# Performance work log

Hardware: AMD Instinct MI355X
Metric: run time of the kernel (lower is better)

Reference implementation:

```python
import jax, jax.numpy as jnp
import numpy as np

B, T, C, H = 4, 2048, 1024, 16
D = C // H  # head dim = 64


def setup_inputs() -> dict:
    key = jax.random.key(0)
    ks = jax.random.split(key, 8)
    s = 1.0 / np.sqrt(C)
    return {
        "x": jax.random.normal(ks[0], (B, T, C), jnp.float32),
        "mask": jax.random.randint(ks[1], (B, T), 0, 2, jnp.int32),
        "Wq": jax.random.normal(ks[2], (C, C), jnp.float32) * s,
        "bq": jnp.zeros((C,), jnp.float32),
        "Wk": jax.random.normal(ks[3], (C, C), jnp.float32) * s,
        "bk": jnp.zeros((C,), jnp.float32),
        "Wv": jax.random.normal(ks[4], (C, C), jnp.float32) * s,
        "bv": jnp.zeros((C,), jnp.float32),
    }


def reference(x, mask, Wq, bq, Wk, bk, Wv, bv):
    # QKV projections (nn.Linear: x @ W.T + b); W stored here as [out,in] -> use W.T
    q = x @ Wq.T + bq
    k = x @ Wk.T + bk
    v = x @ Wv.T + bv
    # split heads: [B,T,C] -> [B,H,T,D]
    q = q.reshape(B, T, H, D).transpose(0, 2, 1, 3)
    k = k.reshape(B, T, H, D).transpose(0, 2, 1, 3)
    v = v.reshape(B, T, H, D).transpose(0, 2, 1, 3)
    # scaled dot-product attention scores [B,H,T,T]
    attn = jnp.einsum("bhqd,bhkd->bhqk", q, k) / jnp.sqrt(jnp.float32(D))
    # additive mask over key positions: attn - inf*(1-mask), expressed stably
    big_neg = jnp.float32(-1e30)
    attn = jnp.where(mask[:, None, None, :] > 0, attn, big_neg)
    attn = jax.nn.softmax(attn, axis=-1)
    # dropout p=0 -> identity
    y = jnp.einsum("bhqk,bhkd->bhqd", attn, v)
    # merge heads: [B,H,T,D] -> [B,T,C]
    return y.transpose(0, 2, 1, 3).reshape(B, T, C)
```

## Files before the change

### kernel.cpp

```cpp
#include <hip/hip_runtime.h>
#include <stdint.h>

#define BB 4
#define TT 2048
#define CC 1024
#define HH 16
#define DD 64
#define MM (BB * TT)

typedef unsigned short u16;
typedef unsigned int   u32;
typedef __attribute__((ext_vector_type(8))) short short8;
typedef _Float16 half8  __attribute__((ext_vector_type(8)));
typedef __fp16   fp16x2 __attribute__((ext_vector_type(2)));
typedef __attribute__((ext_vector_type(4))) float f32x4;
typedef __attribute__((ext_vector_type(4))) unsigned short u16x4;

#if __has_builtin(__builtin_amdgcn_exp2f)
#define EXP2(x) __builtin_amdgcn_exp2f(x)
#else
#define EXP2(x) __expf(0.69314718055994531f * (x))
#endif

__device__ inline u16 f2bf(float f) {
    union { float f; unsigned u; } v; v.f = f;
    unsigned r = 0x7fffu + ((v.u >> 16) & 1u);
    return (u16)((v.u + r) >> 16);
}
__device__ inline u16 f2h(float f) {
    union { _Float16 h; u16 u; } c; c.h = (_Float16)f; return c.u;
}
__device__ inline u32 pkh(float a, float b) {
    union { fp16x2 h; u32 u; } c;
    c.h = __builtin_amdgcn_cvt_pkrtz(a, b);
    return c.u;
}

#define NX (MM * CC / 4)
#define NW (CC * CC / 4)
__global__ void cvt_all(const float* __restrict__ x,  const float* __restrict__ Wq,
                        const float* __restrict__ Wk, const float* __restrict__ Wv,
                        u16* __restrict__ xb, u16* __restrict__ Wb) {
    int i = blockIdx.x * blockDim.x + threadIdx.x;
    const float* src; u16* dst; int j;
    if (i < NX)               { src = x;  dst = xb;                       j = i; }
    else if (i < NX + NW)     { src = Wq; dst = Wb;                       j = i - NX; }
    else if (i < NX + 2 * NW) { src = Wk; dst = Wb + (size_t)CC * CC;     j = i - NX - NW; }
    else if (i < NX + 3 * NW) { src = Wv; dst = Wb + (size_t)2 * CC * CC; j = i - NX - 2 * NW; }
    else return;
    float4 v = ((const float4*)src)[j];
    u16x4 o;
    o.x = f2bf(v.x); o.y = f2bf(v.y); o.z = f2bf(v.z); o.w = f2bf(v.w);
    ((u16x4*)dst)[j] = o;
}

__global__ void qkv_gemm(const u16* __restrict__ xb, const u16* __restrict__ Wb,
                         const float* __restrict__ bq, const float* __restrict__ bk,
                         const float* __restrict__ bv,
                         u16* __restrict__ Qh, u16* __restrict__ Kh, u16* __restrict__ Vt)
{
    const int z = blockIdx.z;
    const u16* W = Wb + (size_t)z * CC * CC;
    const float* bias = (z == 0) ? bq : ((z == 1) ? bk : bv);
    const float scale = (z == 0) ? 0.18033688011112042f : 1.0f;

    __shared__ __align__(16) u16 As[128][32];
    __shared__ __align__(16) u16 Bs[128][32];

    const int tid = threadIdx.x;
    const int l  = tid & 63, w = tid >> 6;
    const int wm = w >> 1,  wn = w & 1;
    const int lr = l & 15,  lq = l >> 4;
    const int m0 = blockIdx.y * 128, n0 = blockIdx.x * 128;

    f32x4 acc[4][4] = {};

    for (int kt = 0; kt < CC; kt += 32) {
        __syncthreads();
        #pragma unroll
        for (int r = 0; r < 2; ++r) {
            int c   = (r * 4 + w) * 64 + l;
            int row = c >> 2, kc = c & 3;
            const u16* ga = xb + (size_t)(m0 + row) * CC + kt + kc * 8;
            __builtin_amdgcn_global_load_lds(
                (const __attribute__((address_space(1))) void*)ga,
                (__attribute__((address_space(3))) void*)(&As[0][0] + (size_t)c * 8), 16, 0, 0);
            const u16* gb = W + (size_t)(n0 + row) * CC + kt + kc * 8;
            __builtin_amdgcn_global_load_lds(
                (const __attribute__((address_space(1))) void*)gb,
                (__attribute__((address_space(3))) void*)(&Bs[0][0] + (size_t)c * 8), 16, 0, 0);
        }
        __syncthreads();

        short8 af[4], bfr[4];
        #pragma unroll
        for (int mi = 0; mi < 4; ++mi)
            af[mi] = *(const short8*)&As[wm * 64 + mi * 16 + lr][lq * 8];
        #pragma unroll
        for (int ni = 0; ni < 4; ++ni)
            bfr[ni] = *(const short8*)&Bs[wn * 64 + ni * 16 + lr][lq * 8];
        #pragma unroll
        for (int mi = 0; mi < 4; ++mi)
            #pragma unroll
            for (int ni = 0; ni < 4; ++ni)
                acc[mi][ni] = __builtin_amdgcn_mfma_f32_16x16x32_bf16(
                    af[mi], bfr[ni], acc[mi][ni], 0, 0, 0);
    }

    if (z == 2) {
        #pragma unroll
        for (int ni = 0; ni < 4; ++ni) {
            int n = n0 + wn * 64 + ni * 16 + lr;
            float bvv = bias[n];
            int h = n >> 6, d = n & 63;
            #pragma unroll
            for (int mi = 0; mi < 4; ++mi) {
                int mbase = m0 + wm * 64 + mi * 16 + lq * 4;
                int b = mbase >> 11, t0 = mbase & (TT - 1);
                u16x4 pkv;
                #pragma unroll
                for (int r = 0; r < 4; ++r)
                    pkv[r] = f2h(acc[mi][ni][r] + bvv);
                *(u16x4*)&Vt[((size_t)(b * HH + h) * DD + d) * TT + t0] = pkv;
            }
        }
    } else {
        u16* out = (z == 0) ? Qh : Kh;
        #pragma unroll
        for (int ni = 0; ni < 4; ++ni) {
            int n = n0 + wn * 64 + ni * 16 + lr;
            float bvv = bias[n];
            int h = n >> 6, d = n & 63;
            #pragma unroll
            for (int mi = 0; mi < 4; ++mi) {
                int mbase = m0 + wm * 64 + mi * 16 + lq * 4;
                #pragma unroll
                for (int r = 0; r < 4; ++r) {
                    int m = mbase + r;
                    int b = m >> 11, t = m & (TT - 1);
                    out[((size_t)(b * HH + h) * TT + t) * DD + d] =
                        f2h((acc[mi][ni][r] + bvv) * scale);
                }
            }
        }
    }
}

__global__ __launch_bounds__(256, 4)
void attn_kernel(const u16* __restrict__ Qh, const u16* __restrict__ Kh,
                 const u16* __restrict__ Vt, const int* __restrict__ mask,
                 float* __restrict__ out)
{
    const int qt = blockIdx.x;
    const int h  = blockIdx.y;
    const int b  = blockIdx.z;
    const int tid = threadIdx.x;
    const int l  = tid & 63, w = tid >> 6;
    const int lr = l & 15,  lq = l >> 4;

    __shared__ __align__(16) u16 Ks[2][2][32][40];
    __shared__ __align__(16) u16 Vs[2][80][40];
    __shared__ __align__(16) u16 Ps[4][32][40];

    const size_t base = (size_t)(b * HH + h) * TT * DD;
    const int q0 = qt * 128 + w * 32;

    half8 qf[2][2];
    #pragma unroll
    for (int qi = 0; qi < 2; ++qi)
        #pragma unroll
        for (int kc = 0; kc < 2; ++kc)
            qf[qi][kc] = *(const half8*)(Qh + base + (size_t)(q0 + qi * 16 + lr) * DD
                                         + kc * 32 + lq * 8);

    const int kk  = tid >> 3, dc = tid & 7;
    const int kh  = dc >> 2, kck = dc & 3;
    const int krow = (kk & 1) * 16 + (kk >> 1);
    u16* k_dst0 = &Ks[0][kh][krow][kck * 8];
    const u16* k_base = Kh + base + (size_t)kk * DD + dc * 8;
    const int vd = tid >> 2, vck = tid & 3;
    u16* v_dst0 = &Vs[0][vd][vck * 8];
    const u16* v_base = Vt + base + (size_t)vd * TT + vck * 8;
    const int2* mrow = (const int2*)(mask + b * TT);

    #pragma unroll
    for (int i = tid; i < 16 * 40; i += 256) {
        (&Vs[0][64][0])[i] = 0x3C00;
        (&Vs[1][64][0])[i] = 0x3C00;
    }

    *(half8*)k_dst0 = *(const half8*)k_base;
    *(half8*)v_dst0 = *(const half8*)v_base;

    f32x4 o[2][5] = {};

    const int NT = TT / 32;
    __syncthreads();

    for (int kt = 0; kt < NT; ++kt) {
        const int p = kt & 1;
        int ktn = (kt + 1 < NT) ? kt + 1 : NT - 1;
        half8 kreg = *(const half8*)(k_base + (size_t)ktn * 32 * DD);
        half8 vreg = *(const half8*)(v_base + ktn * 32);
        int2 mm = mrow[kt * 16 + lr];
        float f0 = (float)mm.x, f1 = (float)mm.y;

        const u16 (*Kp)[32][40] = Ks[p];
        half8 k00 = *(const half8*)&Kp[0][lr][lq * 8];
        half8 k01 = *(const half8*)&Kp[1][lr][lq * 8];
        half8 k10 = *(const half8*)&Kp[0][16 + lr][lq * 8];
        half8 k11 = *(const half8*)&Kp[1][16 + lr][lq * 8];
        f32x4 s0[2], s1[2];
        #pragma unroll
        for (int qi = 0; qi < 2; ++qi) {
            f32x4 z0 = {}, z1 = {};
            z0 = __builtin_amdgcn_mfma_f32_16x16x32_f16(qf[qi][0], k00, z0, 0, 0, 0);
            z0 = __builtin_amdgcn_mfma_f32_16x16x32_f16(qf[qi][1], k01, z0, 0, 0, 0);
            z1 = __builtin_amdgcn_mfma_f32_16x16x32_f16(qf[qi][0], k10, z1, 0, 0, 0);
            z1 = __builtin_amdgcn_mfma_f32_16x16x32_f16(qf[qi][1], k11, z1, 0, 0, 0);
            s0[qi] = z0; s1[qi] = z1;
        }

        #pragma unroll
        for (int qi = 0; qi < 2; ++qi)
            #pragma unroll
            for (int r = 0; r < 4; ++r) {
                float pe = EXP2(s0[qi][r]) * f0;
                float po = EXP2(s1[qi][r]) * f1;
                *(u32*)&Ps[w][qi * 16 + lq * 4 + r][2 * lr] = pkh(pe, po);
            }
        __builtin_amdgcn_sched_barrier(0);
        half8 pf0 = *(const half8*)&Ps[w][lr][lq * 8];
        half8 pf1 = *(const half8*)&Ps[w][16 + lr][lq * 8];

        #pragma unroll
        for (int dg = 0; dg < 5; ++dg) {
            half8 vf = *(const half8*)&Vs[p][dg * 16 + lr][lq * 8];
            o[0][dg] = __builtin_amdgcn_mfma_f32_16x16x32_f16(pf0, vf, o[0][dg], 0, 0, 0);
            o[1][dg] = __builtin_amdgcn_mfma_f32_16x16x32_f16(pf1, vf, o[1][dg], 0, 0, 0);
        }

        *(half8*)(k_dst0 + (p ^ 1) * (2 * 32 * 40)) = kreg;
        *(half8*)(v_dst0 + (p ^ 1) * (80 * 40)) = vreg;
        __syncthreads();
    }

    #pragma unroll
    for (int qi = 0; qi < 2; ++qi)
        #pragma unroll
        for (int r = 0; r < 4; ++r) {
            float inv = 1.f / o[qi][4][r];
            int t = q0 + qi * 16 + lq * 4 + r;
            float* op = out + (size_t)(b * TT + t) * CC + h * DD;
            #pragma unroll
            for (int dg = 0; dg < 4; ++dg)
                op[dg * 16 + lr] = o[qi][dg][r] * inv;
        }
}

extern "C" void kernel_launch(void* const* d_in, const int* in_sizes, int n_in,
                              void* d_out, int out_size, void* d_ws, size_t ws_size,
                              hipStream_t stream) {
    const float* x    = (const float*)d_in[0];
    const int*   mask = (const int*)d_in[1];
    const float* Wq   = (const float*)d_in[2];
    const float* bq   = (const float*)d_in[3];
    const float* Wk   = (const float*)d_in[4];
    const float* bk   = (const float*)d_in[5];
    const float* Wv   = (const float*)d_in[6];
    const float* bv   = (const float*)d_in[7];
    float* out = (float*)d_out;

    u16* xb = (u16*)d_ws;
    u16* Wb = xb + (size_t)MM * CC;
    u16* Qh = Wb + (size_t)3 * CC * CC;
    u16* Kh = Qh + (size_t)MM * CC;
    u16* Vt = Kh + (size_t)MM * CC;

    {
        int total = NX + 3 * NW;
        cvt_all<<<(total + 255) / 256, 256, 0, stream>>>(x, Wq, Wk, Wv, xb, Wb);
    }

    qkv_gemm<<<dim3(CC / 128, MM / 128, 3), 256, 0, stream>>>(xb, Wb, bq, bk, bv, Qh, Kh, Vt);

    attn_kernel<<<dim3(TT / 128, HH, BB), 256, 0, stream>>>(Qh, Kh, Vt, mask, out);
}
```

Measured before the change: 264.8 us.

## Compute transposed scores in registers, drop P LDS round-trip, double query tile

```diff
diff --git a/kernel.cpp b/kernel.cpp
--- a/kernel.cpp
+++ b/kernel.cpp
@@ -15,6 +15,7 @@
 typedef __fp16   fp16x2 __attribute__((ext_vector_type(2)));
 typedef __attribute__((ext_vector_type(4))) float f32x4;
 typedef __attribute__((ext_vector_type(4))) unsigned short u16x4;
+typedef __attribute__((ext_vector_type(4))) unsigned int u32x4;
 
 #if __has_builtin(__builtin_amdgcn_exp2f)
 #define EXP2(x) __builtin_amdgcn_exp2f(x)
@@ -75,6 +76,9 @@
 
     f32x4 acc[4][4] = {};
 
+    const u16* aLDS = (z == 2) ? &As[0][0] : &Bs[0][0];
+    const u16* bLDS = (z == 2) ? &Bs[0][0] : &As[0][0];
+
     for (int kt = 0; kt < CC; kt += 32) {
         __syncthreads();
         #pragma unroll
@@ -95,10 +99,10 @@
         short8 af[4], bfr[4];
         #pragma unroll
         for (int mi = 0; mi < 4; ++mi)
-            af[mi] = *(const short8*)&As[wm * 64 + mi * 16 + lr][lq * 8];
+            af[mi] = *(const short8*)(aLDS + (size_t)(wm * 64 + mi * 16 + lr) * 32 + lq * 8);
         #pragma unroll
         for (int ni = 0; ni < 4; ++ni)
-            bfr[ni] = *(const short8*)&Bs[wn * 64 + ni * 16 + lr][lq * 8];
+            bfr[ni] = *(const short8*)(bLDS + (size_t)(wn * 64 + ni * 16 + lr) * 32 + lq * 8);
         #pragma unroll
         for (int mi = 0; mi < 4; ++mi)
             #pragma unroll
@@ -127,26 +131,26 @@
     } else {
         u16* out = (z == 0) ? Qh : Kh;
         #pragma unroll
-        for (int ni = 0; ni < 4; ++ni) {
-            int n = n0 + wn * 64 + ni * 16 + lr;
-            float bvv = bias[n];
-            int h = n >> 6, d = n & 63;
-            #pragma unroll
-            for (int mi = 0; mi < 4; ++mi) {
-                int mbase = m0 + wm * 64 + mi * 16 + lq * 4;
-                #pragma unroll
-                for (int r = 0; r < 4; ++r) {
-                    int m = mbase + r;
-                    int b = m >> 11, t = m & (TT - 1);
-                    out[((size_t)(b * HH + h) * TT + t) * DD + d] =
-                        f2h((acc[mi][ni][r] + bvv) * scale);
-                }
+        for (int mi = 0; mi < 4; ++mi) {
+            int nb = n0 + wm * 64 + mi * 16 + lq * 4;
+            float4 b4 = *(const float4*)&bias[nb];
+            int h = nb >> 6, d0 = nb & 63;
+            #pragma unroll
+            for (int ni = 0; ni < 4; ++ni) {
+                int m = m0 + wn * 64 + ni * 16 + lr;
+                int b = m >> 11, t = m & (TT - 1);
+                u16x4 pkv;
+                pkv.x = f2h((acc[mi][ni][0] + b4.x) * scale);
+                pkv.y = f2h((acc[mi][ni][1] + b4.y) * scale);
+                pkv.z = f2h((acc[mi][ni][2] + b4.z) * scale);
+                pkv.w = f2h((acc[mi][ni][3] + b4.w) * scale);
+                *(u16x4*)&out[((size_t)(b * HH + h) * TT + t) * DD + d0] = pkv;
             }
         }
     }
 }
 
-__global__ __launch_bounds__(256, 4)
+__global__ __launch_bounds__(256, 2)
 void attn_kernel(const u16* __restrict__ Qh, const u16* __restrict__ Kh,
                  const u16* __restrict__ Vt, const int* __restrict__ mask,
                  float* __restrict__ out)
@@ -158,41 +162,49 @@
     const int l  = tid & 63, w = tid >> 6;
     const int lr = l & 15,  lq = l >> 4;
 
-    __shared__ __align__(16) u16 Ks[2][2][32][40];
+    __shared__ __align__(16) u16 Ks[2][32][72];
     __shared__ __align__(16) u16 Vs[2][80][40];
-    __shared__ __align__(16) u16 Ps[4][32][40];
 
     const size_t base = (size_t)(b * HH + h) * TT * DD;
-    const int q0 = qt * 128 + w * 32;
-
-    half8 qf[2][2];
+    const int q0 = qt * 256 + w * 64;
+
+    half8 qf[4][2];
     #pragma unroll
-    for (int qi = 0; qi < 2; ++qi)
-        #pragma unroll
-        for (int kc = 0; kc < 2; ++kc)
-            qf[qi][kc] = *(const half8*)(Qh + base + (size_t)(q0 + qi * 16 + lr) * DD
-                                         + kc * 32 + lq * 8);
-
-    const int kk  = tid >> 3, dc = tid & 7;
-    const int kh  = dc >> 2, kck = dc & 3;
-    const int krow = (kk & 1) * 16 + (kk >> 1);
-    u16* k_dst0 = &Ks[0][kh][krow][kck * 8];
+    for (int qg = 0; qg < 4; ++qg)
+        #pragma unroll
+        for (int c = 0; c < 2; ++c)
+            qf[qg][c] = *(const half8*)(Qh + base + (size_t)(q0 + qg * 16 + lr) * DD
+                                        + c * 32 + lq * 8);
+
+    const int kk = tid >> 3, dc = tid & 7;
+    u16* k_dst0 = &Ks[0][kk][dc * 8];
     const u16* k_base = Kh + base + (size_t)kk * DD + dc * 8;
     const int vd = tid >> 2, vck = tid & 3;
-    u16* v_dst0 = &Vs[0][vd][vck * 8];
+    const int s0c = ((2 * vck) & 3) * 8 + (vck >> 1) * 4;
+    const int s1c = ((2 * vck + 1) & 3) * 8 + (vck >> 1) * 4;
+    u16* v_dst0a = &Vs[0][vd][s0c];
+    u16* v_dst0b = &Vs[0][vd][s1c];
     const u16* v_base = Vt + base + (size_t)vd * TT + vck * 8;
-    const int2* mrow = (const int2*)(mask + b * TT);
-
-    #pragma unroll
+    const int* mbase_p = mask + b * TT + 4 * lq;
+
     for (int i = tid; i < 16 * 40; i += 256) {
         (&Vs[0][64][0])[i] = 0x3C00;
         (&Vs[1][64][0])[i] = 0x3C00;
     }
 
-    *(half8*)k_dst0 = *(const half8*)k_base;
-    *(half8*)v_dst0 = *(const half8*)v_base;
-
-    f32x4 o[2][5] = {};
+    {
+        half8 k0 = *(const half8*)k_base;
+        half8 v0 = *(const half8*)v_base;
+        *(half8*)k_dst0 = k0;
+        u16x4 va = { (u16)((u32x4&)v0)[0], (u16)(((u32x4&)v0)[0] >> 16),
+                     (u16)((u32x4&)v0)[1], (u16)(((u32x4&)v0)[1] >> 16) };
+        u16x4 vb = { (u16)((u32x4&)v0)[2], (u16)(((u32x4&)v0)[2] >> 16),
+                     (u16)((u32x4&)v0)[3], (u16)(((u32x4&)v0)[3] >> 16) };
+        *(u16x4*)v_dst0a = va;
+        *(u16x4*)v_dst0b = vb;
+    }
+
+    f32x4 o[4][5] = {};
 
     const int NT = TT / 32;
     __syncthreads();
@@ -202,59 +214,68 @@
         int ktn = (kt + 1 < NT) ? kt + 1 : NT - 1;
         half8 kreg = *(const half8*)(k_base + (size_t)ktn * 32 * DD);
         half8 vreg = *(const half8*)(v_base + ktn * 32);
-        int2 mm = mrow[kt * 16 + lr];
-        float f0 = (float)mm.x, f1 = (float)mm.y;
-
-        const u16 (*Kp)[32][40] = Ks[p];
-        half8 k00 = *(const half8*)&Kp[0][lr][lq * 8];
-        half8 k01 = *(const half8*)&Kp[1][lr][lq * 8];
-        half8 k10 = *(const half8*)&Kp[0][16 + lr][lq * 8];
-        half8 k11 = *(const half8*)&Kp[1][16 + lr][lq * 8];
-        f32x4 s0[2], s1[2];
-        #pragma unroll
-        for (int qi = 0; qi < 2; ++qi) {
-            f32x4 z0 = {}, z1 = {};
-            z0 = __builtin_amdgcn_mfma_f32_16x16x32_f16(qf[qi][0], k00, z0, 0, 0, 0);
-            z0 = __builtin_amdgcn_mfma_f32_16x16x32_f16(qf[qi][1], k01, z0, 0, 0, 0);
-            z1 = __builtin_amdgcn_mfma_f32_16x16x32_f16(qf[qi][0], k10, z1, 0, 0, 0);
-            z1 = __builtin_amdgcn_mfma_f32_16x16x32_f16(qf[qi][1], k11, z1, 0, 0, 0);
-            s0[qi] = z0; s1[qi] = z1;
-        }
-
-        #pragma unroll
-        for (int qi = 0; qi < 2; ++qi)
-            #pragma unroll
-            for (int r = 0; r < 4; ++r) {
-                float pe = EXP2(s0[qi][r]) * f0;
-                float po = EXP2(s1[qi][r]) * f1;
-                *(u32*)&Ps[w][qi * 16 + lq * 4 + r][2 * lr] = pkh(pe, po);
+        int4 ma = *(const int4*)(mbase_p + kt * 32);
+        int4 mb = *(const int4*)(mbase_p + kt * 32 + 16);
+
+        half8 kf[2][2];
+        #pragma unroll
+        for (int kg = 0; kg < 2; ++kg)
+            #pragma unroll
+            for (int c = 0; c < 2; ++c)
+                kf[kg][c] = *(const half8*)&Ks[p][kg * 16 + lr][c * 32 + lq * 8];
+
+        f32x4 s[2][4];
+        #pragma unroll
+        for (int kg = 0; kg < 2; ++kg)
+            #pragma unroll
+            for (int qg = 0; qg < 4; ++qg) {
+                f32x4 zz = {};
+                zz = __builtin_amdgcn_mfma_f32_16x16x32_f16(kf[kg][0], qf[qg][0], zz, 0, 0, 0);
+                zz = __builtin_amdgcn_mfma_f32_16x16x32_f16(kf[kg][1], qf[qg][1], zz, 0, 0, 0);
+                s[kg][qg] = zz;
             }
-        __builtin_amdgcn_sched_barrier(0);
-        half8 pf0 = *(const half8*)&Ps[w][lr][lq * 8];
-        half8 pf1 = *(const half8*)&Ps[w][16 + lr][lq * 8];
+
+        float f00 = (float)ma.x, f01 = (float)ma.y, f02 = (float)ma.z, f03 = (float)ma.w;
+        float f10 = (float)mb.x, f11 = (float)mb.y, f12 = (float)mb.z, f13 = (float)mb.w;
+        half8 pf[4];
+        #pragma unroll
+        for (int qg = 0; qg < 4; ++qg) {
+            u32x4 pk;
+            pk[0] = pkh(EXP2(s[0][qg][0]) * f00, EXP2(s[0][qg][1]) * f01);
+            pk[1] = pkh(EXP2(s[0][qg][2]) * f02, EXP2(s[0][qg][3]) * f03);
+            pk[2] = pkh(EXP2(s[1][qg][0]) * f10, EXP2(s[1][qg][1]) * f11);
+            pk[3] = pkh(EXP2(s[1][qg][2]) * f12, EXP2(s[1][qg][3]) * f13);
+            pf[qg] = (half8&)pk;
+        }
 
         #pragma unroll
         for (int dg = 0; dg < 5; ++dg) {
             half8 vf = *(const half8*)&Vs[p][dg * 16 + lr][lq * 8];
-            o[0][dg] = __builtin_amdgcn_mfma_f32_16x16x32_f16(pf0, vf, o[0][dg], 0, 0, 0);
-            o[1][dg] = __builtin_amdgcn_mfma_f32_16x16x32_f16(pf1, vf, o[1][dg], 0, 0, 0);
-        }
-
-        *(half8*)(k_dst0 + (p ^ 1) * (2 * 32 * 40)) = kreg;
-        *(half8*)(v_dst0 + (p ^ 1) * (80 * 40)) = vreg;
+            #pragma unroll
+            for (int qg = 0; qg < 4; ++qg)
+                o[qg][dg] = __builtin_amdgcn_mfma_f32_16x16x32_f16(pf[qg], vf, o[qg][dg], 0, 0, 0);
+        }
+
+        *(half8*)(k_dst0 + (p ^ 1) * (32 * 72)) = kreg;
+        u16x4 va = { (u16)((u32x4&)vreg)[0], (u16)(((u32x4&)vreg)[0] >> 16),
+                     (u16)((u32x4&)vreg)[1], (u16)(((u32x4&)vreg)[1] >> 16) };
+        u16x4 vb = { (u16)((u32x4&)vreg)[2], (u16)(((u32x4&)vreg)[2] >> 16),
+                     (u16)((u32x4&)vreg)[3], (u16)(((u32x4&)vreg)[3] >> 16) };
+        *(u16x4*)(v_dst0a + (p ^ 1) * (80 * 40)) = va;
+        *(u16x4*)(v_dst0b + (p ^ 1) * (80 * 40)) = vb;
         __syncthreads();
     }
 
     #pragma unroll
-    for (int qi = 0; qi < 2; ++qi)
+    for (int qg = 0; qg < 4; ++qg)
         #pragma unroll
         for (int r = 0; r < 4; ++r) {
-            float inv = 1.f / o[qi][4][r];
-            int t = q0 + qi * 16 + lq * 4 + r;
+            float inv = 1.f / o[qg][4][r];
+            int t = q0 + qg * 16 + lq * 4 + r;
             float* op = out + (size_t)(b * TT + t) * CC + h * DD;
             #pragma unroll
             for (int dg = 0; dg < 4; ++dg)
-                op[dg * 16 + lr] = o[qi][dg][r] * inv;
+                op[dg * 16 + lr] = o[qg][dg][r] * inv;
         }
 }
 
@@ -284,5 +305,5 @@
 
     qkv_gemm<<<dim3(CC / 128, MM / 128, 3), 256, 0, stream>>>(xb, Wb, bq, bk, bv, Qh, Kh, Vt);
 
-    attn_kernel<<<dim3(TT / 128, HH, BB), 256, 0, stream>>>(Qh, Kh, Vt, mask, out);
-}
+    attn_kernel<<<dim3(TT / 256, HH, BB), 256, 0, stream>>>(Qh, Kh, Vt, mask, out);
+}
```

Result: faster. 252.6 us (-4.6%).
